# Kernel optimization log

Hardware: AMD Instinct MI355X
Metric: run time of the kernel (lower is better)

## Reference

```python
import jax, jax.numpy as jnp
import numpy as np

V, D, B, L = 433, 120, 4096, 16  # vocab, d_model, batch, seq_len
H4 = 4 * D
LN_EPS = 1e-5


def setup_inputs() -> dict:
    key = jax.random.key(0)
    ks = jax.random.split(key, 12)
    s = 1.0 / np.sqrt(D)  # PyTorch LSTM init range
    u = lambda k, shape: jax.random.uniform(k, shape, jnp.float32, -s, s)
    return {
        "x": jax.random.randint(ks[0], (B, L), 0, V, dtype=jnp.int32),
        "embed": jax.random.normal(ks[1], (V, D), jnp.float32) * 0.02,
        "Wih0": u(ks[2], (H4, D)), "Whh0": u(ks[3], (H4, D)),
        "bih0": u(ks[4], (H4,)), "bhh0": u(ks[5], (H4,)),
        "Wih1": u(ks[6], (H4, D)), "Whh1": u(ks[7], (H4, D)),
        "bih1": u(ks[8], (H4,)), "bhh1": u(ks[9], (H4,)),
        "gamma": jnp.ones((D,), jnp.float32),
        "beta": jnp.zeros((D,), jnp.float32),
    }


def _lstm_layer(x, Wih, Whh, bih, bhh):
    """One LSTM layer, batch_first input [B,L,D] -> [B,L,H]. PyTorch gate order i,f,g,o."""
    b, _, _ = x.shape
    h_dim = Whh.shape[1]
    # Precompute input contribution for all timesteps in one big GEMM.
    xg = jnp.einsum('bld,gd->blg', x, Wih) + bih + bhh  # [B,L,4H]

    def step(carry, g_t):
        h, c = carry
        gates = g_t + h @ Whh.T  # [B,4H]
        i, f, g, o = jnp.split(gates, 4, axis=-1)
        c = jax.nn.sigmoid(f) * c + jax.nn.sigmoid(i) * jnp.tanh(g)
        h = jax.nn.sigmoid(o) * jnp.tanh(c)
        return (h, c), h

    init = (jnp.zeros((b, h_dim), x.dtype), jnp.zeros((b, h_dim), x.dtype))
    _, hs = jax.lax.scan(step, init, jnp.swapaxes(xg, 0, 1))  # [L,B,H]
    return jnp.swapaxes(hs, 0, 1)


def _layernorm(h, gamma, beta):
    mu = jnp.mean(h, axis=-1, keepdims=True)
    var = jnp.mean(jnp.square(h - mu), axis=-1, keepdims=True)
    return (h - mu) / jnp.sqrt(var + LN_EPS) * gamma + beta


def reference(x, embed, Wih0, Whh0, bih0, bhh0, Wih1, Whh1, bih1, bhh1, gamma, beta):
    h = embed[x]                               # [B,L,D] token embedding
    h = _lstm_layer(h, Wih0, Whh0, bih0, bhh0)  # layer 0
    h = _lstm_layer(h, Wih1, Whh1, bih1, bhh1)  # layer 1
    out = _layernorm(h, gamma, beta)
    logits = jnp.einsum('bld,vd->blv', out, embed)  # tied-embedding head (no bias)
    return logits
```

## Files before the change

### kernel.cpp

```cpp
#include <hip/hip_runtime.h>


#define VSZ 433
#define DIM 120
#define BSZ 4096
#define SEQ 16
#define H4  480
#define MTOT (BSZ*SEQ)
#define KP  128
#define NPAD 448
#define TB  16
#define GP  484
#define HP  136

typedef unsigned int   u32;
typedef unsigned short u16;
typedef __attribute__((ext_vector_type(8))) short    v8bf;
typedef __attribute__((ext_vector_type(8))) _Float16 v8h;
typedef __attribute__((ext_vector_type(4))) float    v4f;

__device__ __forceinline__ float bf2f(u16 u){ union{u32 i;float f;}z; z.i=((u32)u)<<16; return z.f; }
__device__ __forceinline__ u16 f2bf(float f){
  union{float f;u32 u;}z; z.f=f;
  u32 u = z.u + 0x7fffu + ((z.u>>16)&1u);
  return (u16)(u>>16);
}
__device__ __forceinline__ u32 packh2(float a, float b){
  union{_Float16 h[2]; u32 u;} z;
  z.h[0] = (_Float16)a; z.h[1] = (_Float16)b;
  return z.u;
}

#define EW_OFF   0u
#define B1S_OFF  831488u
#define EMBP_OFF 833408u
#define HB0_OFF  948096u
#define H1N_OFF  17725312u

__global__ __launch_bounds__(512) void k_ew(const float* __restrict__ embed,
                                            const float* __restrict__ Wih0,
                                            const float* __restrict__ bih0,
                                            const float* __restrict__ bhh0,
                                            float* __restrict__ EW)
{
  __shared__ float e[DIM];
  const int v = blockIdx.x, tid = threadIdx.x;
  if (tid < DIM) e[tid] = embed[v*DIM + tid];
  __syncthreads();
  if (tid < H4) {
    float acc = bih0[tid] + bhh0[tid];
    #pragma unroll
    for (int k0 = 0; k0 < DIM; k0 += 4) {
      float4 w = *(const float4*)(Wih0 + tid*DIM + k0);
      acc = fmaf(e[k0+0], w.x, acc);
      acc = fmaf(e[k0+1], w.y, acc);
      acc = fmaf(e[k0+2], w.z, acc);
      acc = fmaf(e[k0+3], w.w, acc);
    }
    EW[v*H4 + tid] = acc;
  }
}

__global__ __launch_bounds__(256) void k_prep2(const float* __restrict__ embed,
                                               const float* __restrict__ bih1,
                                               const float* __restrict__ bhh1,
                                               u16* __restrict__ embP,
                                               float* __restrict__ b1s)
{
  const int idx = blockIdx.x*256 + threadIdx.x;
  if (idx < NPAD*KP) {
    int n = idx >> 7, k = idx & 127;
    embP[idx] = (n < VSZ && k < DIM) ? f2bf(embed[n*DIM + k]) : (u16)0;
  } else if (idx < NPAD*KP + H4) {
    int g = idx - NPAD*KP;
    b1s[g] = bih1[g] + bhh1[g];
  }
}

__global__ __launch_bounds__(512) void k_rec0(const float* __restrict__ Whh,
                                              const float* __restrict__ EW,
                                              const int* __restrict__ x,
                                              _Float16* __restrict__ hb0)
{
  __shared__ float gLs[TB][GP];
  __shared__ __align__(16) _Float16 hLh[TB][HP];
  __shared__ int xL[TB*SEQ];

  const int tid  = threadIdx.x;
  const int wave = tid >> 6, lane = tid & 63;
  const int cl   = lane & 15, quad = lane >> 4;
  const int b0   = blockIdx.x * TB;

  for (int i = tid; i < TB*SEQ; i += 512) xL[i] = x[b0*SEQ + i];
  for (int i = tid; i < TB*HP; i += 512) (&hLh[0][0])[i] = (_Float16)0.f;
  __syncthreads();

  v8h Bf[4][4];
  #pragma unroll
  for (int i = 0; i < 4; ++i) {
    const int nt = wave*4 + i;
    const bool vld = (nt < 30);
    const int n = vld ? nt*16 + cl : 0;
    #pragma unroll
    for (int kt = 0; kt < 4; ++kt) {
      const int k0 = kt*32 + quad*8;
      v8h f = {0,0,0,0,0,0,0,0};
      if (vld && k0 < DIM) {
        float4 q0 = *(const float4*)(Whh + n*DIM + k0);
        float4 q1 = *(const float4*)(Whh + n*DIM + k0 + 4);
        f[0]=(_Float16)q0.x; f[1]=(_Float16)q0.y; f[2]=(_Float16)q0.z; f[3]=(_Float16)q0.w;
        f[4]=(_Float16)q1.x; f[5]=(_Float16)q1.y; f[6]=(_Float16)q1.z; f[7]=(_Float16)q1.w;
      }
      Bf[i][kt] = f;
    }
  }

  float srcv[4][4];
  auto load_src = [&](int t) {
    #pragma unroll
    for (int i = 0; i < 4; ++i) {
      const int nt = wave*4 + i;
      if (nt < 30) {
        const int n = nt*16 + cl;
        #pragma unroll
        for (int r = 0; r < 4; ++r)
          srcv[i][r] = EW[(size_t)xL[(quad*4 + r)*SEQ + t]*H4 + n];
      }
    }
  };
  load_src(0);

  const int prow = wave*2;
  const bool act = lane < 60;
  const int d0   = lane*2;
  float C[2][2] = {{0.f,0.f},{0.f,0.f}};

  for (int t = 0; t < SEQ; ++t) {
    __syncthreads();
    v8h Af[4];
    #pragma unroll
    for (int kt = 0; kt < 4; ++kt)
      Af[kt] = *(const v8h*)&hLh[cl][kt*32 + quad*8];
    v4f acc[4];
    #pragma unroll
    for (int i = 0; i < 4; ++i) {
      acc[i][0]=srcv[i][0]; acc[i][1]=srcv[i][1];
      acc[i][2]=srcv[i][2]; acc[i][3]=srcv[i][3];
    }
    #pragma unroll
    for (int i = 0; i < 4; ++i)
      if (wave*4 + i < 30) {
        #pragma unroll
        for (int kt = 0; kt < 4; ++kt)
          acc[i] = __builtin_amdgcn_mfma_f32_16x16x32_f16(Af[kt], Bf[i][kt], acc[i], 0, 0, 0);
      }
    if (t + 1 < SEQ) load_src(t + 1);
    #pragma unroll
    for (int i = 0; i < 4; ++i) {
      const int nt = wave*4 + i;
      if (nt < 30) {
        #pragma unroll
        for (int r = 0; r < 4; ++r)
          gLs[quad*4 + r][nt*16 + cl] = acc[i][r];
      }
    }
    __syncthreads();
    #pragma unroll
    for (int rr = 0; rr < 2; ++rr) {
      const int row = prow + rr;
      if (act) {
        const float2 gi = *(const float2*)&gLs[row][d0      ];
        const float2 gf = *(const float2*)&gLs[row][d0 + 120];
        const float2 gg = *(const float2*)&gLs[row][d0 + 240];
        const float2 go = *(const float2*)&gLs[row][d0 + 360];
        float h2[2];
        #pragma unroll
        for (int k = 0; k < 2; ++k) {
          const float vi = k ? gi.y : gi.x, vf = k ? gf.y : gf.x;
          const float vg = k ? gg.y : gg.x, vo = k ? go.y : go.x;
          const float si = 1.f / (1.f + __expf(-vi));
          const float sf = 1.f / (1.f + __expf(-vf));
          const float tg = 1.f - 2.f / (__expf(2.f*vg) + 1.f);
          const float so = 1.f / (1.f + __expf(-vo));
          const float c  = sf * C[rr][k] + si * tg;
          C[rr][k] = c;
          const float tc = 1.f - 2.f / (__expf(2.f*c) + 1.f);
          h2[k] = so * tc;
        }
        *(u32*)&hLh[row][d0] = packh2(h2[0], h2[1]);
        *(u32*)&hb0[((size_t)t*BSZ + b0 + row)*KP + d0] = packh2(h2[0], h2[1]);
      } else {
        *(u32*)&hb0[((size_t)t*BSZ + b0 + row)*KP + 120 + 2*(lane - 60)] = 0u;
      }
    }
  }
}

__global__ __launch_bounds__(512) void k_rec1(const float* __restrict__ Wih1,
                                              const float* __restrict__ Whh1,
                                              const float* __restrict__ b1s,
                                              const _Float16* __restrict__ hb0,
                                              const float* __restrict__ gamma,
                                              const float* __restrict__ beta,
                                              u16* __restrict__ h1n)
{
  __shared__ float gLs[TB][GP];
  __shared__ __align__(16) _Float16 hLh[TB][HP];

  const int tid  = threadIdx.x;
  const int wave = tid >> 6, lane = tid & 63;
  const int cl   = lane & 15, quad = lane >> 4;
  const int b0   = blockIdx.x * TB;

  for (int i = tid; i < TB*HP; i += 512) (&hLh[0][0])[i] = (_Float16)0.f;

  v8h Bi[4][4], Bh[4][4];
  float bias[4];
  #pragma unroll
  for (int i = 0; i < 4; ++i) {
    const int nt = wave*4 + i;
    const bool vld = (nt < 30);
    const int n = vld ? nt*16 + cl : 0;
    bias[i] = vld ? b1s[n] : 0.f;
    #pragma unroll
    for (int kt = 0; kt < 4; ++kt) {
      const int k0 = kt*32 + quad*8;
      v8h fi = {0,0,0,0,0,0,0,0}, fh = {0,0,0,0,0,0,0,0};
      if (vld && k0 < DIM) {
        float4 q0 = *(const float4*)(Wih1 + n*DIM + k0);
        float4 q1 = *(const float4*)(Wih1 + n*DIM + k0 + 4);
        fi[0]=(_Float16)q0.x; fi[1]=(_Float16)q0.y; fi[2]=(_Float16)q0.z; fi[3]=(_Float16)q0.w;
        fi[4]=(_Float16)q1.x; fi[5]=(_Float16)q1.y; fi[6]=(_Float16)q1.z; fi[7]=(_Float16)q1.w;
        float4 p0 = *(const float4*)(Whh1 + n*DIM + k0);
        float4 p1 = *(const float4*)(Whh1 + n*DIM + k0 + 4);
        fh[0]=(_Float16)p0.x; fh[1]=(_Float16)p0.y; fh[2]=(_Float16)p0.z; fh[3]=(_Float16)p0.w;
        fh[4]=(_Float16)p1.x; fh[5]=(_Float16)p1.y; fh[6]=(_Float16)p1.z; fh[7]=(_Float16)p1.w;
      }
      Bi[i][kt] = fi;
      Bh[i][kt] = fh;
    }
  }

  const int prow = wave*2;
  const bool act = lane < 60;
  const int d0   = lane*2;
  float gmm[2] = {0.f, 0.f}, bta[2] = {0.f, 0.f};
  if (act) {
    gmm[0] = gamma[d0]; gmm[1] = gamma[d0+1];
    bta[0] = beta[d0];  bta[1] = beta[d0+1];
  }
  float C[2][2] = {{0.f,0.f},{0.f,0.f}};

  v8h A0n[4];
  #pragma unroll
  for (int kt = 0; kt < 4; ++kt)
    A0n[kt] = *(const v8h*)&hb0[((size_t)0*BSZ + b0 + cl)*KP + kt*32 + quad*8];
  __syncthreads();

  for (int t = 0; t < SEQ; ++t) {
    v8h A0c[4], A1[4];
    #pragma unroll
    for (int kt = 0; kt < 4; ++kt) A0c[kt] = A0n[kt];
    #pragma unroll
    for (int kt = 0; kt < 4; ++kt)
      A1[kt] = *(const v8h*)&hLh[cl][kt*32 + quad*8];
    if (t + 1 < SEQ) {
      #pragma unroll
      for (int kt = 0; kt < 4; ++kt)
        A0n[kt] = *(const v8h*)&hb0[((size_t)(t+1)*BSZ + b0 + cl)*KP + kt*32 + quad*8];
    }
    v4f acc[4];
    #pragma unroll
    for (int i = 0; i < 4; ++i)
      acc[i] = (v4f){bias[i], bias[i], bias[i], bias[i]};
    #pragma unroll
    for (int i = 0; i < 4; ++i)
      if (wave*4 + i < 30) {
        #pragma unroll
        for (int kt = 0; kt < 4; ++kt) {
          acc[i] = __builtin_amdgcn_mfma_f32_16x16x32_f16(A0c[kt], Bi[i][kt], acc[i], 0, 0, 0);
          acc[i] = __builtin_amdgcn_mfma_f32_16x16x32_f16(A1[kt],  Bh[i][kt], acc[i], 0, 0, 0);
        }
      }
    #pragma unroll
    for (int i = 0; i < 4; ++i) {
      const int nt = wave*4 + i;
      if (nt < 30) {
        #pragma unroll
        for (int r = 0; r < 4; ++r)
          gLs[quad*4 + r][nt*16 + cl] = acc[i][r];
      }
    }
    __syncthreads();
    float h2[2][2] = {{0.f,0.f},{0.f,0.f}};
    float s1[2] = {0.f, 0.f}, s2[2] = {0.f, 0.f};
    #pragma unroll
    for (int rr = 0; rr < 2; ++rr) {
      const int row = prow + rr;
      if (act) {
        const float2 gi = *(const float2*)&gLs[row][d0      ];
        const float2 gf = *(const float2*)&gLs[row][d0 + 120];
        const float2 gg = *(const float2*)&gLs[row][d0 + 240];
        const float2 go = *(const float2*)&gLs[row][d0 + 360];
        #pragma unroll
        for (int k = 0; k < 2; ++k) {
          const float vi = k ? gi.y : gi.x, vf = k ? gf.y : gf.x;
          const float vg = k ? gg.y : gg.x, vo = k ? go.y : go.x;
          const float si = 1.f / (1.f + __expf(-vi));
          const float sf = 1.f / (1.f + __expf(-vf));
          const float tg = 1.f - 2.f / (__expf(2.f*vg) + 1.f);
          const float so = 1.f / (1.f + __expf(-vo));
          const float c  = sf * C[rr][k] + si * tg;
          C[rr][k] = c;
          const float tc = 1.f - 2.f / (__expf(2.f*c) + 1.f);
          const float h  = so * tc;
          h2[rr][k] = h;
          s1[rr] += h;
          s2[rr] = fmaf(h, h, s2[rr]);
        }
        *(u32*)&hLh[row][d0] = packh2(h2[rr][0], h2[rr][1]);
      }
    }
    #pragma unroll
    for (int m = 32; m >= 1; m >>= 1) {
      s1[0] += __shfl_xor(s1[0], m);
      s2[0] += __shfl_xor(s2[0], m);
      s1[1] += __shfl_xor(s1[1], m);
      s2[1] += __shfl_xor(s2[1], m);
    }
    #pragma unroll
    for (int rr = 0; rr < 2; ++rr) {
      const int row = prow + rr;
      const float mu = s1[rr] * (1.f/DIM);
      const float var = s2[rr] * (1.f/DIM) - mu*mu;
      const float rs = rsqrtf(var + 1e-5f);
      u16* dst = &h1n[((size_t)(b0 + row)*SEQ + t)*KP];
      if (act) {
        const float v0 = fmaf((h2[rr][0] - mu)*rs, gmm[0], bta[0]);
        const float v1 = fmaf((h2[rr][1] - mu)*rs, gmm[1], bta[1]);
        *(u32*)&dst[d0] = (u32)f2bf(v0) | ((u32)f2bf(v1) << 16);
      } else {
        *(u32*)&dst[120 + 2*(lane - 60)] = 0u;
      }
    }
    __syncthreads();
  }
}

__global__ __launch_bounds__(256) void k_head(const u16* __restrict__ A,
                                              const u16* __restrict__ Bp,
                                              float* __restrict__ out)
{
  const int wv = threadIdx.x >> 6, lane = threadIdx.x & 63;
  const int cl = lane & 15, quad = lane >> 4;
  const int mtb = (blockIdx.x*4 + wv)*4;
  v8bf a[4][4];
  #pragma unroll
  for (int i = 0; i < 4; ++i)
    #pragma unroll
    for (int kt = 0; kt < 4; ++kt)
      a[i][kt] = *(const v8bf*)&A[((size_t)(mtb+i)*16 + cl)*KP + kt*32 + quad*8];
  for (int nt = 0; nt < NPAD/16; ++nt) {
    const int n = nt*16 + cl;
    v8bf bfr[4];
    #pragma unroll
    for (int kt = 0; kt < 4; ++kt)
      bfr[kt] = *(const v8bf*)&Bp[(size_t)n*KP + kt*32 + quad*8];
    #pragma unroll
    for (int i = 0; i < 4; ++i) {
      v4f acc = {0.f, 0.f, 0.f, 0.f};
      #pragma unroll
      for (int kt = 0; kt < 4; ++kt)
        acc = __builtin_amdgcn_mfma_f32_16x16x32_bf16(a[i][kt], bfr[kt], acc, 0, 0, 0);
      if (n < VSZ) {
        #pragma unroll
        for (int r = 0; r < 4; ++r)
          out[(size_t)((mtb+i)*16 + quad*4 + r)*VSZ + n] = acc[r];
      }
    }
  }
}

extern "C" void kernel_launch(void* const* d_in, const int* in_sizes, int n_in,
                              void* d_out, int out_size, void* d_ws, size_t ws_size,
                              hipStream_t stream)
{
  (void)in_sizes; (void)n_in; (void)out_size; (void)ws_size;
  const int*   x     = (const int*)d_in[0];
  const float* embed = (const float*)d_in[1];
  const float* Wih0  = (const float*)d_in[2];
  const float* Whh0  = (const float*)d_in[3];
  const float* bih0  = (const float*)d_in[4];
  const float* bhh0  = (const float*)d_in[5];
  const float* Wih1  = (const float*)d_in[6];
  const float* Whh1  = (const float*)d_in[7];
  const float* bih1  = (const float*)d_in[8];
  const float* bhh1  = (const float*)d_in[9];
  const float* gamma = (const float*)d_in[10];
  const float* beta  = (const float*)d_in[11];

  char* ws = (char*)d_ws;
  float*     EW   = (float*)(ws + EW_OFF);
  float*     b1s  = (float*)(ws + B1S_OFF);
  u16*       embP = (u16*)(ws + EMBP_OFF);
  _Float16*  hb0  = (_Float16*)(ws + HB0_OFF);
  u16*       h1n  = (u16*)(ws + H1N_OFF);

  k_ew   <<<VSZ, 512, 0, stream>>>(embed, Wih0, bih0, bhh0, EW);
  k_prep2<<<226, 256, 0, stream>>>(embed, bih1, bhh1, embP, b1s);
  k_rec0 <<<BSZ/TB, 512, 0, stream>>>(Whh0, EW, x, hb0);
  k_rec1 <<<BSZ/TB, 512, 0, stream>>>(Wih1, Whh1, b1s, hb0, gamma, beta, h1n);
  k_head <<<MTOT/256, 256, 0, stream>>>(h1n, embP, (float*)d_out);
}
```

Before: 286.9 us.

## Fuse tied-embedding logits head into layer-1 recurrent kernel via LDS

```diff
diff --git a/kernel.cpp b/kernel.cpp
--- a/kernel.cpp
+++ b/kernel.cpp
@@ -9,6 +9,7 @@
 #define MTOT (BSZ*SEQ)
 #define KP  128
 #define NPAD 448
+#define NT_HEAD (NPAD/16)
 #define TB  16
 #define GP  484
 #define HP  136
@@ -35,7 +36,6 @@
 #define B1S_OFF  831488u
 #define EMBP_OFF 833408u
 #define HB0_OFF  948096u
-#define H1N_OFF  17725312u
 
 __global__ __launch_bounds__(512) void k_ew(const float* __restrict__ embed,
                                             const float* __restrict__ Wih0,
@@ -202,10 +202,13 @@
                                               const _Float16* __restrict__ hb0,
                                               const float* __restrict__ gamma,
                                               const float* __restrict__ beta,
-                                              u16* __restrict__ h1n)
+                                              const u16* __restrict__ embP,
+                                              float* __restrict__ out)
 {
   __shared__ float gLs[TB][GP];
   __shared__ __align__(16) _Float16 hLh[TB][HP];
+  __shared__ __align__(16) u16 hnL[TB][HP];
+  __shared__ __align__(16) u16 embL[NPAD][HP];
 
   const int tid  = threadIdx.x;
   const int wave = tid >> 6, lane = tid & 63;
@@ -213,6 +216,10 @@
   const int b0   = blockIdx.x * TB;
 
   for (int i = tid; i < TB*HP; i += 512) (&hLh[0][0])[i] = (_Float16)0.f;
+  for (int c = tid; c < NPAD*16; c += 512) {
+    const int rw = c >> 4, c16 = c & 15;
+    *(v8bf*)&embL[rw][c16*8] = *(const v8bf*)&embP[(size_t)rw*KP + c16*8];
+  }
 
   v8h Bi[4][4], Bh[4][4];
   float bias[4];
@@ -334,48 +341,40 @@
       const float mu = s1[rr] * (1.f/DIM);
       const float var = s2[rr] * (1.f/DIM) - mu*mu;
       const float rs = rsqrtf(var + 1e-5f);
-      u16* dst = &h1n[((size_t)(b0 + row)*SEQ + t)*KP];
       if (act) {
         const float v0 = fmaf((h2[rr][0] - mu)*rs, gmm[0], bta[0]);
         const float v1 = fmaf((h2[rr][1] - mu)*rs, gmm[1], bta[1]);
-        *(u32*)&dst[d0] = (u32)f2bf(v0) | ((u32)f2bf(v1) << 16);
+        *(u32*)&hnL[row][d0] = (u32)f2bf(v0) | ((u32)f2bf(v1) << 16);
       } else {
-        *(u32*)&dst[120 + 2*(lane - 60)] = 0u;
+        *(u32*)&hnL[row][120 + 2*(lane - 60)] = 0u;
       }
     }
     __syncthreads();
-  }
-}
-
-__global__ __launch_bounds__(256) void k_head(const u16* __restrict__ A,
-                                              const u16* __restrict__ Bp,
-                                              float* __restrict__ out)
-{
-  const int wv = threadIdx.x >> 6, lane = threadIdx.x & 63;
-  const int cl = lane & 15, quad = lane >> 4;
-  const int mtb = (blockIdx.x*4 + wv)*4;
-  v8bf a[4][4];
-  #pragma unroll
-  for (int i = 0; i < 4; ++i)
-    #pragma unroll
-    for (int kt = 0; kt < 4; ++kt)
-      a[i][kt] = *(const v8bf*)&A[((size_t)(mtb+i)*16 + cl)*KP + kt*32 + quad*8];
-  for (int nt = 0; nt < NPAD/16; ++nt) {
-    const int n = nt*16 + cl;
-    v8bf bfr[4];
-    #pragma unroll
-    for (int kt = 0; kt < 4; ++kt)
-      bfr[kt] = *(const v8bf*)&Bp[(size_t)n*KP + kt*32 + quad*8];
-    #pragma unroll
-    for (int i = 0; i < 4; ++i) {
-      v4f acc = {0.f, 0.f, 0.f, 0.f};
+
+    {
+      v8bf a[4];
       #pragma unroll
       for (int kt = 0; kt < 4; ++kt)
-        acc = __builtin_amdgcn_mfma_f32_16x16x32_bf16(a[i][kt], bfr[kt], acc, 0, 0, 0);
-      if (n < VSZ) {
-        #pragma unroll
-        for (int r = 0; r < 4; ++r)
-          out[(size_t)((mtb+i)*16 + quad*4 + r)*VSZ + n] = acc[r];
+        a[kt] = *(const v8bf*)&hnL[cl][kt*32 + quad*8];
+      #pragma unroll
+      for (int j = 0; j < 4; ++j) {
+        const int nt = wave + 8*j;
+        if (nt < NT_HEAD) {
+          const int n = nt*16 + cl;
+          v8bf bfr[4];
+          #pragma unroll
+          for (int kt = 0; kt < 4; ++kt)
+            bfr[kt] = *(const v8bf*)&embL[n][kt*32 + quad*8];
+          v4f hacc = {0.f, 0.f, 0.f, 0.f};
+          #pragma unroll
+          for (int kt = 0; kt < 4; ++kt)
+            hacc = __builtin_amdgcn_mfma_f32_16x16x32_bf16(a[kt], bfr[kt], hacc, 0, 0, 0);
+          if (n < VSZ) {
+            #pragma unroll
+            for (int r = 0; r < 4; ++r)
+              out[((size_t)(b0 + quad*4 + r)*SEQ + t)*VSZ + n] = hacc[r];
+          }
+        }
       }
     }
   }
@@ -404,11 +403,9 @@
   float*     b1s  = (float*)(ws + B1S_OFF);
   u16*       embP = (u16*)(ws + EMBP_OFF);
   _Float16*  hb0  = (_Float16*)(ws + HB0_OFF);
-  u16*       h1n  = (u16*)(ws + H1N_OFF);
 
   k_ew   <<<VSZ, 512, 0, stream>>>(embed, Wih0, bih0, bhh0, EW);
   k_prep2<<<226, 256, 0, stream>>>(embed, bih1, bhh1, embP, b1s);
   k_rec0 <<<BSZ/TB, 512, 0, stream>>>(Whh0, EW, x, hb0);
-  k_rec1 <<<BSZ/TB, 512, 0, stream>>>(Wih1, Whh1, b1s, hb0, gamma, beta, h1n);
-  k_head <<<MTOT/256, 256, 0, stream>>>(h1n, embP, (float*)d_out);
-}
+  k_rec1 <<<BSZ/TB, 512, 0, stream>>>(Wih1, Whh1, b1s, hb0, gamma, beta, embP, (float*)d_out);
+}
```

Result: faster. 258.3 us (-10.0%).
